# Kernel optimization log

Measured on AMD Instinct MI355X. Metric: run time of the kernel, lower is better.

## Reference

```python
import jax, jax.numpy as jnp
import numpy as np

C = 64        # channels
D = 64        # dense grid side at tensor_stride 1
N = 100000    # active voxels


def _conv3d(x, w, stride, pad):
    # x: (D,D,D,Cin), w: (kd,kh,kw,Cin,Cout) -> (D',D',D',Cout)
    return jax.lax.conv_general_dilated(
        x[None], w, window_strides=(stride,) * 3, padding=pad,
        dimension_numbers=('NDHWC', 'DHWIO', 'NDHWC'))[0]


def _sconv(x, w, b, mask, stride=1, pad='SAME'):
    # Minkowski sparse conv == dense conv on zero-filled grid, restricted to
    # the active output sites (bias only added at active sites).
    return (_conv3d(x, w, stride, pad) + b) * mask


def _forward(coords, coords_ds, feats_c1, feats_ref, w_fuse, b_fuse, w_down, b_down,
             w_conv2, b_conv2, w_p00, b_p00, w_p01, b_p01, w_p10, b_p10,
             w_p11, b_p11, w_p12, b_p12):
    dt = feats_c1.dtype
    Dh = D // 2
    ci, cj, ck = coords[:, 0], coords[:, 1], coords[:, 2]
    di, dj, dk = coords_ds[:, 0], coords_ds[:, 1], coords_ds[:, 2]
    mask = jnp.zeros((D, D, D, 1), dt).at[ci, cj, ck, 0].set(1.0)
    mask_ds = jnp.zeros((Dh, Dh, Dh, 1), dt).at[di, dj, dk, 0].set(1.0)
    fused = jnp.concatenate([feats_c1, feats_ref], axis=1)            # (N, 2C)
    x = jnp.zeros((D, D, D, 2 * C), dt).at[ci, cj, ck].set(fused)
    x = jax.nn.relu(_sconv(x, w_fuse, b_fuse, mask))                  # conv_fuse, k=3 s=1
    x = jax.nn.relu(_sconv(x, w_down, b_down, mask_ds, stride=2, pad='VALID'))  # conv_down1, k=2 s=2
    x = _sconv(x, w_conv2, b_conv2, mask_ds)                          # conv_2, no relu
    for i in range(w_p00.shape[0]):                                   # InceptionResNet x3
        p0 = jax.nn.relu(_sconv(x, w_p00[i], b_p00[i], mask_ds))      # k3 C->C/4
        p0 = _sconv(p0, w_p01[i], b_p01[i], mask_ds)                  # k3 C/4->C/2
        p1 = jax.nn.relu(_sconv(x, w_p10[i], b_p10[i], mask_ds))      # k1 C->C/4
        p1 = jax.nn.relu(_sconv(p1, w_p11[i], b_p11[i], mask_ds))     # k3 C/4->C/4
        p1 = _sconv(p1, w_p12[i], b_p12[i], mask_ds)                  # k1 C/4->C/2
        x = jnp.concatenate([p0, p1], axis=-1) + x                    # cat + residual
    return x[di, dj, dk]                                              # (M, C) sparse output feats


def setup_inputs() -> dict:
    rng = np.random.default_rng(0)
    flat = rng.choice(D ** 3, size=N, replace=False)                  # unique occupied voxels
    coords = np.stack(np.unravel_index(flat, (D, D, D)), axis=1).astype(np.int32)
    coords_ds = np.unique(coords // 2, axis=0).astype(np.int32)       # stride-2 active set
    key = jax.random.key(0)
    ks = iter(jax.random.split(key, 40))

    def W(shape, fan_in):
        return jax.random.normal(next(ks), shape, jnp.float32) / np.float32(np.sqrt(fan_in))

    def B(shape):
        return jax.random.normal(next(ks), shape, jnp.float32) * 0.01

    L = 3  # res blocks
    return dict(
        coords=jnp.asarray(coords), coords_ds=jnp.asarray(coords_ds),
        feats_c1=jax.random.normal(next(ks), (N, C), jnp.float32),
        feats_ref=jax.random.normal(next(ks), (N, C), jnp.float32),
        w_fuse=W((3, 3, 3, 2 * C, C), 27 * 2 * C), b_fuse=B((C,)),
        w_down=W((2, 2, 2, C, C), 8 * C), b_down=B((C,)),
        w_conv2=W((3, 3, 3, C, C), 27 * C), b_conv2=B((C,)),
        w_p00=W((L, 3, 3, 3, C, C // 4), 27 * C), b_p00=B((L, C // 4)),
        w_p01=W((L, 3, 3, 3, C // 4, C // 2), 27 * C // 4), b_p01=B((L, C // 2)),
        w_p10=W((L, 1, 1, 1, C, C // 4), C), b_p10=B((L, C // 4)),
        w_p11=W((L, 3, 3, 3, C // 4, C // 4), 27 * C // 4), b_p11=B((L, C // 4)),
        w_p12=W((L, 1, 1, 1, C // 4, C // 2), C // 4), b_p12=B((L, C // 2)),
    )


def reference(coords, coords_ds, feats_c1, feats_ref, w_fuse, b_fuse, w_down, b_down,
              w_conv2, b_conv2, w_p00, b_p00, w_p01, b_p01, w_p10, b_p10,
              w_p11, b_p11, w_p12, b_p12):
    return _forward(coords, coords_ds, feats_c1, feats_ref, w_fuse, b_fuse, w_down,
                    b_down, w_conv2, b_conv2, w_p00, b_p00, w_p01, b_p01, w_p10,
                    b_p10, w_p11, b_p11, w_p12, b_p12)
```

## Files before the change

kernel.cpp:

```cpp
#include <hip/hip_runtime.h>

#define GD 64
#define GDS 32

typedef _Float16 f16;
typedef __attribute__((ext_vector_type(8))) _Float16 f16x8;
typedef __attribute__((ext_vector_type(4))) float f32x4;

#define GLOAD_LDS16(SRC, DST)                                                        \
    __builtin_amdgcn_global_load_lds(                                                \
        (const __attribute__((address_space(1))) unsigned int*)(const void*)(SRC),   \
        (__attribute__((address_space(3))) unsigned int*)(void*)(DST), 16, 0, 0)

__global__ __launch_bounds__(256) void init_kernel(int* __restrict__ idx_grid,
                                                   unsigned char* __restrict__ ds_mask,
                                                   f16* __restrict__ zrow,
                                                   f16* __restrict__ f1z) {
    int i = blockIdx.x * 256 + threadIdx.x;
    if (i < GD * GD * GD) idx_grid[i] = -1;
    if (i < GDS * GDS * GDS) ds_mask[i] = 0;
    if (i < 128) zrow[i] = (f16)0.f;
    if (i < 64) f1z[i] = (f16)0.f;
}

__global__ __launch_bounds__(256) void scatter_kernel(const int* __restrict__ coords, int N,
                                                      const int* __restrict__ coords_ds, int M,
                                                      int* __restrict__ idx_grid,
                                                      unsigned char* __restrict__ ds_mask) {
    int i = blockIdx.x * 256 + threadIdx.x;
    if (i < N) {
        int a = coords[i * 3], b = coords[i * 3 + 1], c = coords[i * 3 + 2];
        idx_grid[(a * GD + b) * GD + c] = i;
    }
    if (i < M) {
        int a = coords_ds[i * 3], b = coords_ds[i * 3 + 1], c = coords_ds[i * 3 + 2];
        ds_mask[(a * GDS + b) * GDS + c] = 1;
    }
}

__global__ __launch_bounds__(256) void count_kernel(const int* __restrict__ idx_grid,
                                                    int* __restrict__ cnt) {
    __shared__ int c;
    if (threadIdx.x == 0) c = 0;
    __syncthreads();
    int s = blockIdx.x * 256 + threadIdx.x;
    bool act = idx_grid[s] >= 0;
    unsigned long long m = __ballot(act);
    if ((threadIdx.x & 63) == 0) atomicAdd(&c, __popcll(m));
    __syncthreads();
    if (threadIdx.x == 0) cnt[blockIdx.x] = c;
}

__global__ __launch_bounds__(1024) void prefix_kernel(const int* __restrict__ cnt,
                                                      int* __restrict__ off) {
    __shared__ int s[1024];
    int t = threadIdx.x;
    int v0 = cnt[t];
    s[t] = v0;
    __syncthreads();
    for (int d = 1; d < 1024; d <<= 1) {
        int v = 0;
        if (t >= d) v = s[t - d];
        __syncthreads();
        s[t] += v;
        __syncthreads();
    }
    off[t] = s[t] - v0;
}

__global__ __launch_bounds__(256) void emit_kernel(int* __restrict__ idx_grid,
                                                   const int* __restrict__ off,
                                                   int* __restrict__ sites,
                                                   int* __restrict__ perm) {
    int tid = threadIdx.x, bid = blockIdx.x;
    int s = bid * 256 + tid;
    int orig = idx_grid[s];
    bool act = orig >= 0;
    unsigned long long m = __ballot(act);
    int lane = tid & 63, wv = tid >> 6;
    __shared__ int wcnt[4];
    if (lane == 0) wcnt[wv] = __popcll(m);
    __syncthreads();
    int base = off[bid];
    for (int w = 0; w < wv; ++w) base += wcnt[w];
    int rank = __popcll(m & ((1ull << lane) - 1ull));
    if (act) {
        int q = base + rank;
        sites[q] = s;
        perm[q] = orig;
        idx_grid[s] = q;
    }
}

__global__ __launch_bounds__(256) void pack_kernel(
    const float* __restrict__ wf, const float* __restrict__ wd, const float* __restrict__ wc2,
    const float* __restrict__ wp00, const float* __restrict__ wp01, const float* __restrict__ wp10,
    const float* __restrict__ wp11, const float* __restrict__ wp12, const float* __restrict__ bp00,
    const float* __restrict__ bp01, const float* __restrict__ bp10, const float* __restrict__ bp11,
    int L, f16* __restrict__ wc1, f16* __restrict__ wdnh, f16* __restrict__ wc2h,
    f16* __restrict__ wfA, f16* __restrict__ wfB, f16* __restrict__ w12h, float* __restrict__ bA,
    float* __restrict__ bB) {
    int i = blockIdx.x * 256 + threadIdx.x;
    int n;
    n = 27 * 8192;
    if (i < n) {
        int tap = i >> 13, oc = (i >> 7) & 63, ic = i & 127;
        wc1[i] = (f16)wf[(tap * 128 + ic) * 64 + oc];
        return;
    }
    i -= n;
    n = 8 * 4096;
    if (i < n) {
        int t = i >> 12, oc = (i >> 6) & 63, ic = i & 63;
        wdnh[i] = (f16)wd[(t * 64 + ic) * 64 + oc];
        return;
    }
    i -= n;
    n = 27 * 4096;
    if (i < n) {
        int tap = i >> 12, oc = (i >> 6) & 63, ic = i & 63;
        wc2h[i] = (f16)wc2[(tap * 64 + ic) * 64 + oc];
        return;
    }
    i -= n;
    n = L * 27 * 2048;
    if (i < n) {
        int l = i / (27 * 2048), r = i - l * 27 * 2048;
        int tap = r >> 11, oc = (r >> 6) & 31, ic = r & 63;
        float v = 0.f;
        if (oc < 16) v = wp00[(((size_t)l * 27 + tap) * 64 + ic) * 16 + oc];
        else if (tap == 13) v = wp10[((size_t)l * 64 + ic) * 16 + (oc - 16)];
        wfA[i] = (f16)v;
        return;
    }
    i -= n;
    n = L * 27 * 1536;
    if (i < n) {
        int l = i / (27 * 1536), r = i - l * 27 * 1536;
        int tap = r / 1536, q = r - tap * 1536;
        int oc = q >> 5, ic = q & 31;
        float v = 0.f;
        if (oc < 32) {
            if (ic < 16) v = wp01[(((size_t)l * 27 + tap) * 16 + ic) * 32 + oc];
        } else {
            if (ic >= 16) v = wp11[(((size_t)l * 27 + tap) * 16 + (ic - 16)) * 16 + (oc - 32)];
        }
        wfB[i] = (f16)v;
        return;
    }
    i -= n;
    n = L * 512;
    if (i < n) {
        int l = i >> 9, q = i & 511, oc = q >> 4, ic = q & 15;
        w12h[i] = (f16)wp12[((size_t)l * 16 + ic) * 32 + oc];
        return;
    }
    i -= n;
    n = L * 32;
    if (i < n) {
        int l = i >> 5, oc = i & 31;
        bA[i] = (oc < 16) ? bp00[l * 16 + oc] : bp10[l * 16 + oc - 16];
        return;
    }
    i -= n;
    n = L * 48;
    if (i < n) {
        int l = i / 48, c = i - l * 48;
        bB[i] = (c < 32) ? bp01[l * 32 + c] : bp11[l * 16 + (c - 32)];
    }
}

__global__ __launch_bounds__(256) void fusef_kernel(const float* __restrict__ fc1,
                                                    const float* __restrict__ fref,
                                                    const int* __restrict__ perm, int N,
                                                    f16* __restrict__ feats) {
    int i = blockIdx.x * 256 + threadIdx.x;
    if (i < (N + 1) * 128) {
        int q = i >> 7, c = i & 127;
        float v = 0.f;
        if (q < N) {
            int p = perm[q];
            v = (c < 64) ? fc1[p * 64 + c] : fref[p * 64 + c - 64];
        }
        feats[i] = (f16)v;
    }
}

__global__ __launch_bounds__(256) void conv1_pipe(const int* __restrict__ sites,
                                                  const int* __restrict__ idx_grid, int N,
                                                  const f16* __restrict__ featsB,
                                                  const f16* __restrict__ wc1,
                                                  const float* __restrict__ bias,
                                                  f16* __restrict__ out ) {
    __shared__ f16 xb[2][64 * 128];
    __shared__ f16 wb[2][64 * 128];
    __shared__ int nbr[64 * 27];
    const int tid = threadIdx.x;
    const int nwg = gridDim.x, orig = blockIdx.x;
    const int qq = nwg >> 3, rr2 = nwg & 7;
    const int xcd = orig & 7, sub = orig >> 3;
    const int wg = (xcd < rr2 ? xcd * (qq + 1) : rr2 * (qq + 1) + (xcd - rr2) * qq) + sub;
    const int q0 = wg * 64;

    for (int t = tid; t < 64 * 27; t += 256) {
        int p = t / 27, tap = t - p * 27;
        int q = q0 + p, nb = N;
        if (q < N) {
            int s = sites[q];
            int i = (s >> 12) + tap / 9 - 1;
            int j = ((s >> 6) & 63) + (tap / 3) % 3 - 1;
            int k = (s & 63) + tap % 3 - 1;
            if ((unsigned)i < 64u && (unsigned)j < 64u && (unsigned)k < 64u) {
                int r = idx_grid[(i << 12) + (j << 6) + k];
                if (r >= 0) nb = r;
            }
        }
        nbr[t] = nb;
    }
    __syncthreads();

    const int lane = tid & 63, wid = tid >> 6;
    const int l16 = lane & 15, lq = lane >> 4;
    const int m0 = (wid >> 1) * 32, n0 = (wid & 1) * 32;

    auto STAGE = [&](int tap, int buf) {
#pragma unroll
        for (int r = 0; r < 4; ++r) {
            int slot = r * 256 + tid;
            int row = slot >> 4, cl = slot & 15;
            int c = cl ^ (row & 7);
            const f16* src = featsB + (size_t)nbr[row * 27 + tap] * 128 + c * 8;
            GLOAD_LDS16(src, &xb[buf][0] + (size_t)(r * 256 + (tid & ~63)) * 8);
        }
#pragma unroll
        for (int r = 0; r < 4; ++r) {
            int slot = r * 256 + tid;
            int row = slot >> 4, cl = slot & 15;
            int c = cl ^ (row & 7);
            const f16* src = wc1 + (size_t)((tap * 64 + row) * 128 + c * 8);
            GLOAD_LDS16(src, &wb[buf][0] + (size_t)(r * 256 + (tid & ~63)) * 8);
        }
    };

    f32x4 acc[2][2] = {};
    STAGE(0, 0);
    STAGE(1, 1);
    for (int tap = 0; tap < 27; ++tap) {
        if (tap < 26) {
            asm volatile("s_waitcnt vmcnt(8)" ::: "memory");
        } else {
            asm volatile("s_waitcnt vmcnt(0)" ::: "memory");
        }
        __builtin_amdgcn_sched_barrier(0);
        __builtin_amdgcn_s_barrier();

        const f16* xp = &xb[tap & 1][0];
        const f16* wp = &wb[tap & 1][0];
        f16x8 a[2][4], b[2][4];
#pragma unroll
        for (int mi = 0; mi < 2; ++mi) {
            int row = m0 + mi * 16 + l16;
#pragma unroll
            for (int ks = 0; ks < 4; ++ks)
                a[mi][ks] =
                    *(const f16x8*)(xp + (size_t)row * 128 + (size_t)(((ks * 4 + lq) ^ (row & 7)) * 8));
        }
#pragma unroll
        for (int ni = 0; ni < 2; ++ni) {
            int col = n0 + ni * 16 + l16;
#pragma unroll
            for (int ks = 0; ks < 4; ++ks)
                b[ni][ks] =
                    *(const f16x8*)(wp + (size_t)col * 128 + (size_t)(((ks * 4 + lq) ^ (col & 7)) * 8));
        }
#pragma unroll
        for (int mi = 0; mi < 2; ++mi)
#pragma unroll
            for (int ni = 0; ni < 2; ++ni)
#pragma unroll
                for (int ks = 0; ks < 4; ++ks)
                    acc[mi][ni] = __builtin_amdgcn_mfma_f32_16x16x32_f16(a[mi][ks], b[ni][ks],
                                                                         acc[mi][ni], 0, 0, 0);
        asm volatile("s_waitcnt lgkmcnt(0)" ::: "memory");
        __builtin_amdgcn_sched_barrier(0);
        __builtin_amdgcn_s_barrier();
        if (tap + 2 < 27) STAGE(tap + 2, tap & 1);
    }

#pragma unroll
    for (int ni = 0; ni < 2; ++ni) {
        int col = n0 + ni * 16 + l16;
        float bv = bias[col];
#pragma unroll
        for (int mi = 0; mi < 2; ++mi) {
#pragma unroll
            for (int j = 0; j < 4; ++j) {
                int q = q0 + m0 + mi * 16 + lq * 4 + j;
                if (q < N) {
                    float v = acc[mi][ni][j] + bv;
                    out[(size_t)q * 64 + col] = (f16)(v > 0.f ? v : 0.f);
                }
            }
        }
    }
}

__global__ __launch_bounds__(512) void down_mfma(const f16* __restrict__ feats1h, int N,
                                                 const int* __restrict__ idx_grid,
                                                 const f16* __restrict__ wdn,
                                                 const float* __restrict__ bias,
                                                 const unsigned char* __restrict__ mask,
                                                 f16* __restrict__ out ) {
    __shared__ f16 xs[2][128 * 64];
    __shared__ int nbr[128 * 8];
    const int tid = threadIdx.x;
    const int s0 = blockIdx.x * 128;
    for (int t = tid; t < 128 * 8; t += 512) {
        int sl = t >> 3, tp = t & 7;
        int s = s0 + sl;
        int i = s >> 10, j = (s >> 5) & 31, k = s & 31;
        int ci = 2 * i + (tp >> 2), cj = 2 * j + ((tp >> 1) & 1), ck = 2 * k + (tp & 1);
        int r = idx_grid[(ci * GD + cj) * GD + ck];
        nbr[t] = (r >= 0) ? r : N;
    }
    __syncthreads();
    auto stage = [&](int tp, int buf) {
#pragma unroll
        for (int rr = 0; rr < 2; ++rr) {
            int slot = rr * 512 + tid;
            int row = slot >> 3, cl = slot & 7;
            int c = cl ^ (row & 7);
            const f16* src = feats1h + (size_t)nbr[row * 8 + tp] * 64 + c * 8;
            f16* dst = &xs[buf][0] + (size_t)(rr * 512 + (tid & ~63)) * 8;
            GLOAD_LDS16(src, dst);
        }
    };
    const int lane = tid & 63, wid = tid >> 6;
    const int l16 = lane & 15, lq = lane >> 4;
    const int wm = wid >> 1, wn = wid & 1;
    const int m0 = wm * 32, n0 = wn * 32;
    f32x4 acc[2][2] = {};
    stage(0, 0);
    __syncthreads();
    for (int tp = 0; tp < 8; ++tp) {
        if (tp < 7) stage(tp + 1, (tp + 1) & 1);
        const f16* xb = &xs[tp & 1][0];
        f16x8 a[2][2], bfr[2][2];
#pragma unroll
        for (int mi = 0; mi < 2; ++mi) {
            int row = m0 + mi * 16 + l16;
#pragma unroll
            for (int ks = 0; ks < 2; ++ks) {
                int ch = ks * 4 + lq;
                a[mi][ks] = *(const f16x8*)(xb + (size_t)row * 64 + (ch ^ (row & 7)) * 8);
            }
        }
#pragma unroll
        for (int ni = 0; ni < 2; ++ni) {
            int col = n0 + ni * 16 + l16;
#pragma unroll
            for (int ks = 0; ks < 2; ++ks)
                bfr[ni][ks] =
                    *(const f16x8*)(wdn + (size_t)((tp * 64 + col) * 64 + (ks * 4 + lq) * 8));
        }
#pragma unroll
        for (int mi = 0; mi < 2; ++mi)
#pragma unroll
            for (int ni = 0; ni < 2; ++ni)
#pragma unroll
                for (int ks = 0; ks < 2; ++ks)
                    acc[mi][ni] = __builtin_amdgcn_mfma_f32_16x16x32_f16(a[mi][ks], bfr[ni][ks],
                                                                         acc[mi][ni], 0, 0, 0);
        __syncthreads();
    }
#pragma unroll
    for (int mi = 0; mi < 2; ++mi) {
        int m = m0 + mi * 16 + lq * 4;
        int site = s0 + m;
        unsigned mword = *(const unsigned*)(mask + site);
#pragma unroll
        for (int ni = 0; ni < 2; ++ni) {
            int col = n0 + ni * 16 + l16;
            float bv = bias[col];
#pragma unroll
            for (int j = 0; j < 4; ++j) {
                float v = 0.f;
                if ((mword >> (8 * j)) & 255) {
                    v = acc[mi][ni][j] + bv;
                    v = v > 0.f ? v : 0.f;
                }
                out[(size_t)(site + j) * 64 + col] = (f16)v;
            }
        }
    }
}

template <int CIN, int COUT, int NW, int RELUFROM>
__global__ __launch_bounds__(512) void dconv_kernel(const f16* __restrict__ x,
                                                    const f16* __restrict__ wp,
                                                    const float* __restrict__ bias,
                                                    const unsigned char* __restrict__ mask,
                                                    const f16* __restrict__ zrow,
                                                    f16* __restrict__ out, int ostr) {
    constexpr int NCH = CIN / 8;
    constexpr int PSLOT = 34 * NCH;
    constexpr int STOT = 18 * PSLOT;
    constexpr int RNDS = (STOT + 511) / 512;
    constexpr int MW = 8 / NW;
    constexpr int WM = 128 / MW, WN = COUT / NW;
    constexpr int FM = WM / 16, FN = WN / 16, KS = CIN / 32;
    __shared__ f16 xs[RNDS * 512 * 8];

    const int tid = threadIdx.x;
    const int bid = blockIdx.x;
    const int i0 = bid >> 3, j0 = (bid & 7) * 4;

    for (int rr = 0; rr < RNDS; ++rr) {
        int slot = rr * 512 + tid;
        int p = slot / PSLOT;
        int rem = slot - p * PSLOT;
        int r = rem / NCH;
        int cl = rem - r * NCH;
        int c = cl ^ (r & (NCH - 1));
        int gi = i0 + p / 6 - 1, gj = j0 + p % 6 - 1, gk = r - 1;
        bool ok = (slot < STOT) && ((unsigned)gi < 32u) && ((unsigned)gj < 32u) &&
                  ((unsigned)gk < 32u);
        const f16* src = ok ? (x + (size_t)(((gi * 32 + gj) * 32 + gk) * CIN + c * 8)) : zrow;
        f16* dst = xs + (size_t)(rr * 512 + (tid & ~63)) * 8;
        GLOAD_LDS16(src, dst);
    }
    __syncthreads();

    const int lane = tid & 63, wid = tid >> 6;
    const int l16 = lane & 15, lq = lane >> 4;
    const int wm = wid / NW, wn = wid - wm * NW;
    const int m0 = wm * WM, n0 = wn * WN;

    f32x4 acc[FM][FN] = {};

    for (int tap = 0; tap < 27; ++tap) {
        int di = tap / 9 - 1, dj = (tap / 3) % 3 - 1, dk = tap % 3 - 1;
        f16x8 a[FM][KS], bfr[FN][KS];
#pragma unroll
        for (int mi = 0; mi < FM; ++mi) {
            int m = m0 + mi * 16 + l16;
            int pj = m >> 5, k = m & 31;
            int p = (di + 1) * 6 + (pj + dj + 1);
            int r = k + dk + 1;
#pragma unroll
            for (int ks = 0; ks < KS; ++ks) {
                int ch = ks * 4 + lq;
                a[mi][ks] =
                    *(const f16x8*)(xs + (size_t)(p * PSLOT + r * NCH + (ch ^ (r & (NCH - 1)))) * 8);
            }
        }
#pragma unroll
        for (int ni = 0; ni < FN; ++ni) {
            int col = n0 + ni * 16 + l16;
#pragma unroll
            for (int ks = 0; ks < KS; ++ks)
                bfr[ni][ks] =
                    *(const f16x8*)(wp + (size_t)((tap * COUT + col) * CIN + (ks * 4 + lq) * 8));
        }
#pragma unroll
        for (int mi = 0; mi < FM; ++mi)
#pragma unroll
            for (int ni = 0; ni < FN; ++ni)
#pragma unroll
                for (int ks = 0; ks < KS; ++ks)
                    acc[mi][ni] = __builtin_amdgcn_mfma_f32_16x16x32_f16(a[mi][ks], bfr[ni][ks],
                                                                         acc[mi][ni], 0, 0, 0);
    }

#pragma unroll
    for (int mi = 0; mi < FM; ++mi) {
        int m = m0 + mi * 16 + lq * 4;
        int pj = m >> 5, k = m & 31;
        int gsite = ((i0 * 32) + (j0 + pj)) * 32 + k;
        unsigned mword = *(const unsigned*)(mask + gsite);
#pragma unroll
        for (int ni = 0; ni < FN; ++ni) {
            int col = n0 + ni * 16 + l16;
            float bv = bias[col];
#pragma unroll
            for (int j = 0; j < 4; ++j) {
                float v = 0.f;
                if ((mword >> (8 * j)) & 255) {
                    v = acc[mi][ni][j] + bv;
                    if (col >= RELUFROM) v = v > 0.f ? v : 0.f;
                }
                out[(size_t)(gsite + j) * ostr + col] = (f16)v;
            }
        }
    }
}

template <typename OUTT>
__global__ __launch_bounds__(256) void tail_kernel(const f16* __restrict__ ph,
                                                   const f16* __restrict__ xh,
                                                   const f16* __restrict__ w12,
                                                   const float* __restrict__ b12,
                                                   const unsigned char* __restrict__ mask,
                                                   OUTT* __restrict__ y ) {
    __shared__ float ws[512];
    __shared__ float bs[32];
    int tid = threadIdx.x;
    ws[tid] = (float)w12[tid];
    ws[tid + 256] = (float)w12[tid + 256];
    if (tid < 32) bs[tid] = b12[tid];
    __syncthreads();
    int g = tid >> 6, lane = tid & 63;
    int site = blockIdx.x * 64 + lane;
    const f16x8* pr = (const f16x8*)(ph + (size_t)site * 64);
    const f16x8* xr = (const f16x8*)(xh + (size_t)site * 64);
    float yv[16];
    int col0;
    if (g < 2) {
        col0 = g * 16;
        f16x8 p0 = pr[g * 2], p1 = pr[g * 2 + 1];
        f16x8 x0 = xr[g * 2], x1 = xr[g * 2 + 1];
#pragma unroll
        for (int j = 0; j < 8; ++j) {
            yv[j] = (float)p0[j] + (float)x0[j];
            yv[8 + j] = (float)p1[j] + (float)x1[j];
        }
    } else {
        int oc0 = (g - 2) * 16;
        col0 = 32 + oc0;
        f16x8 u0 = pr[4], u1 = pr[5];
        float u[16];
#pragma unroll
        for (int j = 0; j < 8; ++j) {
            u[j] = (float)u0[j];
            u[8 + j] = (float)u1[j];
        }
        f16x8 x0 = xr[4 + (g - 2) * 2], x1 = xr[5 + (g - 2) * 2];
        bool mk = mask[site] != 0;
#pragma unroll
        for (int oc = 0; oc < 16; ++oc) {
            float s = 0.f;
#pragma unroll
            for (int ic = 0; ic < 16; ++ic) s += u[ic] * ws[(oc0 + oc) * 16 + ic];
            float p1v = mk ? (s + bs[oc0 + oc]) : 0.f;
            yv[oc] = p1v + (float)((oc < 8) ? x0[oc] : x1[oc - 8]);
        }
    }
#pragma unroll
    for (int j = 0; j < 16; ++j) y[(size_t)site * 64 + col0 + j] = (OUTT)yv[j];
}

__global__ __launch_bounds__(256) void gather_kernel(const float* __restrict__ x,
                                                     const int* __restrict__ coords_ds, int M,
                                                     float* __restrict__ out) {
    int i = blockIdx.x * 256 + threadIdx.x;
    if (i < M * 64) {
        int m = i >> 6, oc = i & 63;
        int a = coords_ds[m * 3], b = coords_ds[m * 3 + 1], c = coords_ds[m * 3 + 2];
        out[i] = x[((size_t)((a * GDS + b) * GDS + c) << 6) + oc];
    }
}

extern "C" void kernel_launch(void* const* d_in, const int* in_sizes, int n_in,
                              void* d_out, int out_size, void* d_ws, size_t ws_size,
                              hipStream_t stream) {
    const int* coords = (const int*)d_in[0];
    const int* coords_ds = (const int*)d_in[1];
    const float* fc1 = (const float*)d_in[2];
    const float* fref = (const float*)d_in[3];
    const float* w_fuse = (const float*)d_in[4];
    const float* b_fuse = (const float*)d_in[5];
    const float* w_down = (const float*)d_in[6];
    const float* b_down = (const float*)d_in[7];
    const float* w_conv2 = (const float*)d_in[8];
    const float* b_conv2 = (const float*)d_in[9];
    const float* w_p00 = (const float*)d_in[10];
    const float* b_p00 = (const float*)d_in[11];
    const float* w_p01 = (const float*)d_in[12];
    const float* b_p01 = (const float*)d_in[13];
    const float* w_p10 = (const float*)d_in[14];
    const float* b_p10 = (const float*)d_in[15];
    const float* w_p11 = (const float*)d_in[16];
    const float* b_p11 = (const float*)d_in[17];
    const float* w_p12 = (const float*)d_in[18];
    const float* b_p12 = (const float*)d_in[19];

    const int N = in_sizes[0] / 3;
    const int M = in_sizes[1] / 3;
    const int L = in_sizes[10] / (27 * 64 * 16);
    const int NSITES = GDS * GDS * GDS;

    size_t off = 0;
    auto alloc = [&](size_t bytes) {
        void* p = (char*)d_ws + off;
        off += (bytes + 255) & ~(size_t)255;
        return p;
    };
    int* idx_grid = (int*)alloc((size_t)GD * GD * GD * 4);
    unsigned char* ds_mask = (unsigned char*)alloc(NSITES);
    f16* zrow = (f16*)alloc(256);
    int* chunk_cnt = (int*)alloc(1024 * 4);
    int* chunk_off = (int*)alloc(1024 * 4);
    int* sites = (int*)alloc((size_t)N * 4);
    int* perm = (int*)alloc((size_t)N * 4);
    f16* featsB = (f16*)alloc((size_t)(N + 1) * 128 * 2);
    f16* feats1h = (f16*)alloc((size_t)(N + 1) * 64 * 2);
    f16* xdown = (f16*)alloc((size_t)NSITES * 64 * 2);
    f16* x0 = (f16*)alloc((size_t)NSITES * 64 * 2);
    f16* y1 = (f16*)alloc((size_t)NSITES * 64 * 2);
    f16* y2 = (f16*)alloc((size_t)NSITES * 64 * 2);
    f16* thh = (f16*)alloc((size_t)NSITES * 32 * 2);
    f16* ph = (f16*)alloc((size_t)NSITES * 64 * 2);
    float* xF = (float*)alloc((size_t)NSITES * 64 * 4);
    f16* wc1 = (f16*)alloc((size_t)27 * 8192 * 2);
    f16* wdnh = (f16*)alloc((size_t)8 * 4096 * 2);
    f16* wc2h = (f16*)alloc((size_t)27 * 4096 * 2);
    f16* wfA = (f16*)alloc((size_t)L * 27 * 2048 * 2);
    f16* wfB = (f16*)alloc((size_t)L * 27 * 1536 * 2);
    f16* w12h = (f16*)alloc((size_t)L * 512 * 2);
    float* bA = (float*)alloc((size_t)L * 32 * 4);
    float* bB = (float*)alloc((size_t)L * 48 * 4);
    (void)ws_size;

    float* out = (float*)d_out;
    (void)out_size;
    (void)n_in;

    init_kernel<<<(GD * GD * GD + 255) / 256, 256, 0, stream>>>(idx_grid, ds_mask, zrow,
                                                                feats1h + (size_t)N * 64);
    {
        int mx = N > M ? N : M;
        scatter_kernel<<<(mx + 255) / 256, 256, 0, stream>>>(coords, N, coords_ds, M, idx_grid,
                                                             ds_mask);
    }
    count_kernel<<<1024, 256, 0, stream>>>(idx_grid, chunk_cnt);
    prefix_kernel<<<1, 1024, 0, stream>>>(chunk_cnt, chunk_off);
    emit_kernel<<<1024, 256, 0, stream>>>(idx_grid, chunk_off, sites, perm);
    {
        int tot = 27 * 8192 + 8 * 4096 + 27 * 4096 + L * 27 * 2048 + L * 27 * 1536 + L * 512 +
                  L * 32 + L * 48;
        pack_kernel<<<(tot + 255) / 256, 256, 0, stream>>>(
            w_fuse, w_down, w_conv2, w_p00, w_p01, w_p10, w_p11, w_p12, b_p00, b_p01, b_p10, b_p11,
            L, wc1, wdnh, wc2h, wfA, wfB, w12h, bA, bB);
    }
    fusef_kernel<<<((N + 1) * 128 + 255) / 256, 256, 0, stream>>>(fc1, fref, perm, N, featsB);

    conv1_pipe<<<(N + 63) / 64, 256, 0, stream>>>(sites, idx_grid, N, featsB, wc1, b_fuse,
                                                  feats1h);
    down_mfma<<<NSITES / 128, 512, 0, stream>>>(feats1h, N, idx_grid, wdnh, b_down, ds_mask,
                                                xdown);
    dconv_kernel<64, 64, 2, 64>
        <<<256, 512, 0, stream>>>(xdown, wc2h, b_conv2, ds_mask, zrow, x0, 64);

    f16* x = x0;
    for (int l = 0; l < L; ++l) {
        dconv_kernel<64, 32, 2, 0>
            <<<256, 512, 0, stream>>>(x, wfA + (size_t)l * 27 * 2048, bA + l * 32, ds_mask, zrow,
                                      thh, 32);
        dconv_kernel<32, 48, 1, 32>
            <<<256, 512, 0, stream>>>(thh, wfB + (size_t)l * 27 * 1536, bB + l * 48, ds_mask, zrow,
                                      ph, 64);
        if (l < L - 1) {
            f16* yn = (l == 0) ? y1 : y2;
            tail_kernel<f16><<<NSITES / 64, 256, 0, stream>>>(ph, x, w12h + (size_t)l * 512,
                                                              b_p12 + l * 32, ds_mask, yn);
            x = yn;
        } else {
            tail_kernel<float><<<NSITES / 64, 256, 0, stream>>>(ph, x, w12h + (size_t)l * 512,
                                                                b_p12 + l * 32, ds_mask, xF);
        }
    }

    gather_kernel<<<(M * 64 + 255) / 256, 256, 0, stream>>>(xF, coords_ds, M, out);
}
```

Measured before the change: 323.0 us.

## Stage conv weights through double-buffered LDS and widen conv1 swizzle to 16

The down-sampling and dense sub-manifold conv kernels used to read their weight fragments straight from global memory. They now copy each tap's weights into a double-buffered LDS tile with async global-to-LDS loads, using explicit vmcnt waits and barriers in a two-stage pipeline. The first conv kernel's LDS XOR swizzle changes from row&7 to row&15 (lane index) so its 128-channel rows cover all 16 chunks and bank conflicts drop. The cost is extra LDS use, two barriers per tap and hand-tuned waitcnt counts that must match the number of outstanding loads.

```diff
diff --git a/kernel.cpp b/kernel.cpp
--- a/kernel.cpp
+++ b/kernel.cpp
@@ -228,7 +228,7 @@
         for (int r = 0; r < 4; ++r) {
             int slot = r * 256 + tid;
             int row = slot >> 4, cl = slot & 15;
-            int c = cl ^ (row & 7);
+            int c = cl ^ (row & 15);
             const f16* src = featsB + (size_t)nbr[row * 27 + tap] * 128 + c * 8;
             GLOAD_LDS16(src, &xb[buf][0] + (size_t)(r * 256 + (tid & ~63)) * 8);
         }
@@ -236,7 +236,7 @@
         for (int r = 0; r < 4; ++r) {
             int slot = r * 256 + tid;
             int row = slot >> 4, cl = slot & 15;
-            int c = cl ^ (row & 7);
+            int c = cl ^ (row & 15);
             const f16* src = wc1 + (size_t)((tap * 64 + row) * 128 + c * 8);
             GLOAD_LDS16(src, &wb[buf][0] + (size_t)(r * 256 + (tid & ~63)) * 8);
         }
@@ -263,7 +263,7 @@
 #pragma unroll
             for (int ks = 0; ks < 4; ++ks)
                 a[mi][ks] =
-                    *(const f16x8*)(xp + (size_t)row * 128 + (size_t)(((ks * 4 + lq) ^ (row & 7)) * 8));
+                    *(const f16x8*)(xp + (size_t)row * 128 + (size_t)((((ks * 4 + lq) ^ l16)) * 8));
         }
 #pragma unroll
         for (int ni = 0; ni < 2; ++ni) {
@@ -271,7 +271,7 @@
 #pragma unroll
             for (int ks = 0; ks < 4; ++ks)
                 b[ni][ks] =
-                    *(const f16x8*)(wp + (size_t)col * 128 + (size_t)(((ks * 4 + lq) ^ (col & 7)) * 8));
+                    *(const f16x8*)(wp + (size_t)col * 128 + (size_t)((((ks * 4 + lq) ^ l16)) * 8));
         }
 #pragma unroll
         for (int mi = 0; mi < 2; ++mi)
@@ -312,6 +312,7 @@
                                                  const unsigned char* __restrict__ mask,
                                                  f16* __restrict__ out ) {
     __shared__ f16 xs[2][128 * 64];
+    __shared__ f16 wl[2][512 * 8];
     __shared__ int nbr[128 * 8];
     const int tid = threadIdx.x;
     const int s0 = blockIdx.x * 128;
@@ -324,27 +325,41 @@
         nbr[t] = (r >= 0) ? r : N;
     }
     __syncthreads();
-    auto stage = [&](int tp, int buf) {
+    auto STAGEX = [&](int tp, int buf) {
 #pragma unroll
         for (int rr = 0; rr < 2; ++rr) {
             int slot = rr * 512 + tid;
             int row = slot >> 3, cl = slot & 7;
             int c = cl ^ (row & 7);
             const f16* src = feats1h + (size_t)nbr[row * 8 + tp] * 64 + c * 8;
-            f16* dst = &xs[buf][0] + (size_t)(rr * 512 + (tid & ~63)) * 8;
-            GLOAD_LDS16(src, dst);
-        }
+            GLOAD_LDS16(src, &xs[buf][0] + (size_t)(rr * 512 + (tid & ~63)) * 8);
+        }
+    };
+    auto STAGEW = [&](int tp, int buf) {
+        int row = tid >> 3, cl = tid & 7;
+        int c = cl ^ (row & 7);
+        const f16* src = wdn + (size_t)((tp * 64 + row) * 64 + c * 8);
+        GLOAD_LDS16(src, &wl[buf][0] + (size_t)(tid & ~63) * 8);
     };
     const int lane = tid & 63, wid = tid >> 6;
     const int l16 = lane & 15, lq = lane >> 4;
     const int wm = wid >> 1, wn = wid & 1;
     const int m0 = wm * 32, n0 = wn * 32;
     f32x4 acc[2][2] = {};
-    stage(0, 0);
-    __syncthreads();
+    STAGEX(0, 0);
+    STAGEW(0, 0);
+    STAGEX(1, 1);
+    STAGEW(1, 1);
     for (int tp = 0; tp < 8; ++tp) {
-        if (tp < 7) stage(tp + 1, (tp + 1) & 1);
-        const f16* xb = &xs[tp & 1][0];
+        if (tp < 7) {
+            asm volatile("s_waitcnt vmcnt(3)" ::: "memory");
+        } else {
+            asm volatile("s_waitcnt vmcnt(0)" ::: "memory");
+        }
+        __builtin_amdgcn_sched_barrier(0);
+        __builtin_amdgcn_s_barrier();
+        const f16* xbp = &xs[tp & 1][0];
+        const f16* wbp = &wl[tp & 1][0];
         f16x8 a[2][2], bfr[2][2];
 #pragma unroll
         for (int mi = 0; mi < 2; ++mi) {
@@ -352,16 +367,17 @@
 #pragma unroll
             for (int ks = 0; ks < 2; ++ks) {
                 int ch = ks * 4 + lq;
-                a[mi][ks] = *(const f16x8*)(xb + (size_t)row * 64 + (ch ^ (row & 7)) * 8);
+                a[mi][ks] = *(const f16x8*)(xbp + (size_t)row * 64 + (ch ^ (row & 7)) * 8);
             }
         }
 #pragma unroll
         for (int ni = 0; ni < 2; ++ni) {
             int col = n0 + ni * 16 + l16;
 #pragma unroll
-            for (int ks = 0; ks < 2; ++ks)
-                bfr[ni][ks] =
-                    *(const f16x8*)(wdn + (size_t)((tp * 64 + col) * 64 + (ks * 4 + lq) * 8));
+            for (int ks = 0; ks < 2; ++ks) {
+                int ch = ks * 4 + lq;
+                bfr[ni][ks] = *(const f16x8*)(wbp + (size_t)col * 64 + (ch ^ (col & 7)) * 8);
+            }
         }
 #pragma unroll
         for (int mi = 0; mi < 2; ++mi)
@@ -371,7 +387,13 @@
                 for (int ks = 0; ks < 2; ++ks)
                     acc[mi][ni] = __builtin_amdgcn_mfma_f32_16x16x32_f16(a[mi][ks], bfr[ni][ks],
                                                                          acc[mi][ni], 0, 0, 0);
-        __syncthreads();
+        asm volatile("s_waitcnt lgkmcnt(0)" ::: "memory");
+        __builtin_amdgcn_sched_barrier(0);
+        __builtin_amdgcn_s_barrier();
+        if (tp + 2 < 8) {
+            STAGEX(tp + 2, tp & 1);
+            STAGEW(tp + 2, tp & 1);
+        }
     }
 #pragma unroll
     for (int mi = 0; mi < 2; ++mi) {
@@ -409,7 +431,9 @@
     constexpr int MW = 8 / NW;
     constexpr int WM = 128 / MW, WN = COUT / NW;
     constexpr int FM = WM / 16, FN = WN / 16, KS = CIN / 32;
+    constexpr int WSLOTS = COUT * NCH;
     __shared__ f16 xs[RNDS * 512 * 8];
+    __shared__ f16 wl[2][512 * 8];
 
     const int tid = threadIdx.x;
     const int bid = blockIdx.x;
@@ -429,7 +453,14 @@
         f16* dst = xs + (size_t)(rr * 512 + (tid & ~63)) * 8;
         GLOAD_LDS16(src, dst);
     }
-    __syncthreads();
+    auto STAGEW = [&](int tap, int buf) {
+        int row = tid / NCH, cl = tid % NCH;
+        int c = cl ^ (row & (NCH - 1));
+        const f16* src = (tid < WSLOTS) ? (wp + (size_t)((tap * COUT + row) * CIN + c * 8)) : wp;
+        GLOAD_LDS16(src, &wl[buf][0] + (size_t)(tid & ~63) * 8);
+    };
+    STAGEW(0, 0);
+    STAGEW(1, 1);
 
     const int lane = tid & 63, wid = tid >> 6;
     const int l16 = lane & 15, lq = lane >> 4;
@@ -439,7 +470,16 @@
     f32x4 acc[FM][FN] = {};
 
     for (int tap = 0; tap < 27; ++tap) {
+        if (tap < 26) {
+            asm volatile("s_waitcnt vmcnt(1)" ::: "memory");
+        } else {
+            asm volatile("s_waitcnt vmcnt(0)" ::: "memory");
+        }
+        __builtin_amdgcn_sched_barrier(0);
+        __builtin_amdgcn_s_barrier();
+
         int di = tap / 9 - 1, dj = (tap / 3) % 3 - 1, dk = tap % 3 - 1;
+        const f16* wbp = &wl[tap & 1][0];
         f16x8 a[FM][KS], bfr[FN][KS];
 #pragma unroll
         for (int mi = 0; mi < FM; ++mi) {
@@ -458,9 +498,11 @@
         for (int ni = 0; ni < FN; ++ni) {
             int col = n0 + ni * 16 + l16;
 #pragma unroll
-            for (int ks = 0; ks < KS; ++ks)
+            for (int ks = 0; ks < KS; ++ks) {
+                int ch = ks * 4 + lq;
                 bfr[ni][ks] =
-                    *(const f16x8*)(wp + (size_t)((tap * COUT + col) * CIN + (ks * 4 + lq) * 8));
+                    *(const f16x8*)(wbp + (size_t)(col * NCH + (ch ^ (col & (NCH - 1)))) * 8);
+            }
         }
 #pragma unroll
         for (int mi = 0; mi < FM; ++mi)
@@ -470,6 +512,10 @@
                 for (int ks = 0; ks < KS; ++ks)
                     acc[mi][ni] = __builtin_amdgcn_mfma_f32_16x16x32_f16(a[mi][ks], bfr[ni][ks],
                                                                          acc[mi][ni], 0, 0, 0);
+        asm volatile("s_waitcnt lgkmcnt(0)" ::: "memory");
+        __builtin_amdgcn_sched_barrier(0);
+        __builtin_amdgcn_s_barrier();
+        if (tap + 2 < 27) STAGEW(tap + 2, tap & 1);
     }
 
 #pragma unroll
```

After: 292.3 us. 1.11x faster.
